# Kernel optimization log

Hardware: AMD Instinct MI355X
Metric: run time of the kernel (lower is better)

The kernel has to match this reference:

```python
import jax, jax.numpy as jnp
import numpy as np

N_NODES = 40000
N_EDGES = 640000
D_IN = 128
D_OUT = 128


def setup_inputs() -> dict:
    key = jax.random.key(0)
    k1, k2, k3 = jax.random.split(key, 3)
    x = jax.random.normal(k1, (N_NODES, D_IN), dtype=jnp.float32)
    W = jax.random.normal(k2, (D_IN, D_OUT), dtype=jnp.float32) / np.sqrt(D_IN)
    b = jnp.zeros((D_OUT,), dtype=jnp.float32)
    edge_index = jax.random.randint(k3, (2, N_EDGES), 0, N_NODES, dtype=jnp.int64)
    return {"x": x, "W": W, "b": b, "edge_index": edge_index}


def reference(x, W, b, edge_index):
    src, dst = edge_index[0], edge_index[1]
    n = x.shape[0]
    # asymmetric normalization: 1 / out-degree(src), inf -> 0
    deg = jax.ops.segment_sum(jnp.ones_like(src, dtype=x.dtype), src, num_segments=n)
    deg_inv = jnp.where(deg > 0, 1.0 / deg, 0.0)
    # GCNConv (add_self_loops=False, normalize=False): h = x @ W; msg_e = w_e * h[src_e]
    h = x @ W  # [N, D_OUT]
    msg = h[src] * deg_inv[src][:, None]  # [E, D_OUT] gather-weighted messages
    out = jax.ops.segment_sum(msg, dst, num_segments=n) + b  # scatter-add to dst
    return out
```

## Files before the change

kernel.cpp:

```cpp
#include <hip/hip_runtime.h>

#define N_NODES 40000
#define D 128
#define N_EDGES 640000
#define CAP 64
#define NSLICE 32
#define SLICE_E 20000
#define SLICE_E4 5000
#define HALF_BINS 20000
#define HALF_W 10000
#define WROW 20000
#define SRCHIST_BLKS 64
#define BIN_BLKS 625
#define GEMM_BLKS 625
#define XPAD 132

typedef __attribute__((ext_vector_type(8))) short short8_t;
typedef __attribute__((ext_vector_type(4))) float float4_t;

static __device__ __forceinline__ unsigned short f2bf(float f) {
  unsigned u = __float_as_uint(f);
  return (unsigned short)((u + 0x7fffu + ((u >> 16) & 1u)) >> 16);
}
static __device__ __forceinline__ float bf2f(unsigned short h) {
  return __uint_as_float(((unsigned)h) << 16);
}

__global__ __launch_bounds__(256) void k_prep(const float* __restrict__ W,
                                              unsigned short* __restrict__ Wb,
                                              int* __restrict__ cnt_dst) {
  const int bid = blockIdx.x;
  const int tid = threadIdx.x;
  if (bid < 64) {
    const int g = bid * 256 + tid;
    const int j = g & 7;
    const int lane = (g >> 3) & 63;
    const int q = (g >> 9) & 3;
    const int t = g >> 11;
    const int k = q * 32 + (lane >> 4) * 8 + j;
    const int d = t * 16 + (lane & 15);
    Wb[g] = f2bf(W[k * D + d]);
  } else {
    const int i = (bid - 64) * 256 + tid;
    if (i < N_NODES) cnt_dst[i] = 0;
  }
}

__global__ __launch_bounds__(256) void k_fused(
    const float* __restrict__ x, const unsigned short* __restrict__ Wb,
    const int* __restrict__ src, const int* __restrict__ dst,
    int* __restrict__ cnt_dst, unsigned* __restrict__ slabS,
    unsigned short* __restrict__ bucket, unsigned short* __restrict__ hb) {
  __shared__ unsigned smem[10240];
  const int bid = blockIdx.x;
  const int tid = threadIdx.x;

  if (bid < SRCHIST_BLKS) {
    const int b = bid >> 1;
    const int h = bid & 1;
    for (int i = tid; i < HALF_W; i += 256) smem[i] = 0;
    __syncthreads();
    const int4* p4 = (const int4*)(src + b * SLICE_E);
    const unsigned lo = (unsigned)(h * HALF_BINS);
    for (int it = tid; it < SLICE_E4; it += 256) {
      const int4 v = p4[it];
      unsigned u;
      u = (unsigned)v.x - lo; if (u < HALF_BINS) atomicAdd(&smem[u >> 1], 1u << ((u & 1) * 16));
      u = (unsigned)v.y - lo; if (u < HALF_BINS) atomicAdd(&smem[u >> 1], 1u << ((u & 1) * 16));
      u = (unsigned)v.z - lo; if (u < HALF_BINS) atomicAdd(&smem[u >> 1], 1u << ((u & 1) * 16));
      u = (unsigned)v.w - lo; if (u < HALF_BINS) atomicAdd(&smem[u >> 1], 1u << ((u & 1) * 16));
    }
    __syncthreads();
    unsigned* row = slabS + (size_t)b * WROW + h * HALF_W;
    for (int i = tid; i < HALF_W; i += 256) row[i] = smem[i];
    return;
  }

  const int t = bid - SRCHIST_BLKS;

  if (t & 1) {
    const int cid = t >> 1;
    const int e0 = (cid * 256 + tid) * 4;
    const int4 s4 = *(const int4*)(src + e0);
    const int4 d4 = *(const int4*)(dst + e0);
    int r;
    r = atomicAdd(&cnt_dst[d4.x], 1);
    if (r < CAP) bucket[(size_t)d4.x * CAP + r] = (unsigned short)s4.x;
    r = atomicAdd(&cnt_dst[d4.y], 1);
    if (r < CAP) bucket[(size_t)d4.y * CAP + r] = (unsigned short)s4.y;
    r = atomicAdd(&cnt_dst[d4.z], 1);
    if (r < CAP) bucket[(size_t)d4.z * CAP + r] = (unsigned short)s4.z;
    r = atomicAdd(&cnt_dst[d4.w], 1);
    if (r < CAP) bucket[(size_t)d4.w * CAP + r] = (unsigned short)s4.w;
    return;
  }

  const int gid = t >> 1;
  const int n0 = gid * 64;
  const int w = tid >> 6;
  const int lane = tid & 63;

  float* xl = (float*)smem;
  {
    const float4* xg = (const float4*)(x + (size_t)n0 * D);
#pragma unroll
    for (int j = 0; j < 8; ++j) {
      const int idx = tid + j * 256;
      const int row = idx >> 5;
      const int c4 = idx & 31;
      ((float4*)(xl + row * XPAD))[c4] = xg[idx];
    }
  }
  __syncthreads();

  short8_t afrag[4];
  {
    const float* ap0 = xl + (w * 16 + (lane & 15)) * XPAD + (lane >> 4) * 8;
#pragma unroll
    for (int q = 0; q < 4; ++q) {
      const float* ap = ap0 + q * 32;
      const float4 v0 = *(const float4*)ap;
      const float4 v1 = *(const float4*)(ap + 4);
      short8_t a;
      a[0] = (short)f2bf(v0.x); a[1] = (short)f2bf(v0.y);
      a[2] = (short)f2bf(v0.z); a[3] = (short)f2bf(v0.w);
      a[4] = (short)f2bf(v1.x); a[5] = (short)f2bf(v1.y);
      a[6] = (short)f2bf(v1.z); a[7] = (short)f2bf(v1.w);
      afrag[q] = a;
    }
  }

  const int orow = n0 + w * 16 + (lane >> 4) * 4;
  const int ocolbase = lane & 15;
#pragma unroll
  for (int t8 = 0; t8 < 8; ++t8) {
    float4_t acc = {0.f, 0.f, 0.f, 0.f};
#pragma unroll
    for (int q = 0; q < 4; ++q) {
      const short8_t bfrag =
          *(const short8_t*)(Wb + ((size_t)(t8 * 4 + q) * 64 + lane) * 8);
      acc = __builtin_amdgcn_mfma_f32_16x16x32_bf16(afrag[q], bfrag, acc, 0, 0, 0);
    }
    const int col = t8 * 16 + ocolbase;
#pragma unroll
    for (int r = 0; r < 4; ++r)
      hb[(size_t)(orow + r) * D + col] = f2bf(acc[r]);
  }
}

__global__ __launch_bounds__(256) void k_colsum_src(
    const unsigned* __restrict__ slabS, float* __restrict__ dinv) {
  const int w = blockIdx.x * 256 + threadIdx.x;
  if (w >= WROW) return;
  unsigned run = 0;
#pragma unroll 8
  for (int b = 0; b < NSLICE; ++b) run += slabS[(size_t)b * WROW + w];
  const unsigned lo = run & 0xFFFFu;
  const unsigned hi = run >> 16;
  dinv[2 * w] = lo ? 1.0f / (float)lo : 0.0f;
  dinv[2 * w + 1] = hi ? 1.0f / (float)hi : 0.0f;
}

__global__ __launch_bounds__(256) void k_gather(
    const int* __restrict__ cnt_dst, const float* __restrict__ dinv,
    const unsigned short* __restrict__ bucket,
    const unsigned short* __restrict__ hb,
    const float* __restrict__ b, float* __restrict__ out) {
  const int tid = threadIdx.x;
  const int node = blockIdx.x * 8 + (tid >> 5);
  const int lane = tid & 31;

  int len = cnt_dst[node];
  if (len > CAP) len = CAP;
  const unsigned short* bk = bucket + (size_t)node * CAP;

  float4 a0 = {0.f, 0.f, 0.f, 0.f};
  float4 a1 = {0.f, 0.f, 0.f, 0.f};
  float4 a2 = {0.f, 0.f, 0.f, 0.f};
  float4 a3 = {0.f, 0.f, 0.f, 0.f};

  int j = 0;
  for (; j + 3 < len; j += 4) {
    const int s0 = bk[j + 0];
    const int s1 = bk[j + 1];
    const int s2 = bk[j + 2];
    const int s3 = bk[j + 3];
    const float f0 = dinv[s0];
    const float f1 = dinv[s1];
    const float f2 = dinv[s2];
    const float f3 = dinv[s3];
    ushort4 u0 = ((const ushort4*)(hb + (size_t)s0 * D))[lane];
    ushort4 u1 = ((const ushort4*)(hb + (size_t)s1 * D))[lane];
    ushort4 u2 = ((const ushort4*)(hb + (size_t)s2 * D))[lane];
    ushort4 u3 = ((const ushort4*)(hb + (size_t)s3 * D))[lane];
    a0.x += f0 * bf2f(u0.x); a0.y += f0 * bf2f(u0.y); a0.z += f0 * bf2f(u0.z); a0.w += f0 * bf2f(u0.w);
    a1.x += f1 * bf2f(u1.x); a1.y += f1 * bf2f(u1.y); a1.z += f1 * bf2f(u1.z); a1.w += f1 * bf2f(u1.w);
    a2.x += f2 * bf2f(u2.x); a2.y += f2 * bf2f(u2.y); a2.z += f2 * bf2f(u2.z); a2.w += f2 * bf2f(u2.w);
    a3.x += f3 * bf2f(u3.x); a3.y += f3 * bf2f(u3.y); a3.z += f3 * bf2f(u3.z); a3.w += f3 * bf2f(u3.w);
  }
  for (; j < len; ++j) {
    const int s0 = bk[j];
    const float f0 = dinv[s0];
    ushort4 u0 = ((const ushort4*)(hb + (size_t)s0 * D))[lane];
    a0.x += f0 * bf2f(u0.x); a0.y += f0 * bf2f(u0.y); a0.z += f0 * bf2f(u0.z); a0.w += f0 * bf2f(u0.w);
  }

  const float4 bias = ((const float4*)b)[lane];
  float4 v;
  v.x = bias.x + (a0.x + a1.x) + (a2.x + a3.x);
  v.y = bias.y + (a0.y + a1.y) + (a2.y + a3.y);
  v.z = bias.z + (a0.z + a1.z) + (a2.z + a3.z);
  v.w = bias.w + (a0.w + a1.w) + (a2.w + a3.w);
  ((float4*)(out + (size_t)node * D))[lane] = v;
}

extern "C" void kernel_launch(void* const* d_in, const int* in_sizes, int n_in,
                              void* d_out, int out_size, void* d_ws, size_t ws_size,
                              hipStream_t stream) {
  const float* x = (const float*)d_in[0];
  const float* W = (const float*)d_in[1];
  const float* b = (const float*)d_in[2];
  const int* ei = (const int*)d_in[3];
  const int* src = ei;
  const int* dst = ei + N_EDGES;
  float* out = (float*)d_out;

  char* ws = (char*)d_ws;
  int* cnt_dst = (int*)(ws + 0);
  float* dinv = (float*)(ws + 160000);
  unsigned* slabS = (unsigned*)(ws + 320000);
  unsigned short* Wb = (unsigned short*)(ws + 2880000);
  unsigned short* bucket = (unsigned short*)(ws + 2912768);
  unsigned short* hb = (unsigned short*)(ws + 8032768);

  k_prep<<<221, 256, 0, stream>>>(W, Wb, cnt_dst);
  k_fused<<<SRCHIST_BLKS + BIN_BLKS + GEMM_BLKS, 256, 0, stream>>>(
      x, Wb, src, dst, cnt_dst, slabS, bucket, hb);
  k_colsum_src<<<79, 256, 0, stream>>>(slabS, dinv);
  k_gather<<<5000, 256, 0, stream>>>(cnt_dst, dinv, bucket, hb, b, out);
}
```

Measured before the change: 76.76 us.

## Replace global atomic dst bucketing with two-pass counting sort and LDS buckets

Replaces per-edge global atomics into a per-node bucket array with a coarse counting sort. Edges are first histogrammed per 128-node key, then prefix-scanned and scattered into a packed edge array. The gather kernel then builds each group's buckets in LDS before aggregating. This removes contended global atomics and the large bucket array, at the cost of two extra kernel launches and serialized scans. It also cuts the gather kernel's parallelism to 313 blocks that each loop over 128 nodes.

```diff
diff --git a/kernel.cpp b/kernel.cpp
--- a/kernel.cpp
+++ b/kernel.cpp
@@ -4,14 +4,17 @@
 #define D 128
 #define N_EDGES 640000
 #define CAP 64
+#define GRP 128
+#define NKEY 313
+#define P1TILE 2048
+#define P1BLKS 313
 #define NSLICE 32
 #define SLICE_E 20000
 #define SLICE_E4 5000
 #define HALF_BINS 20000
 #define HALF_W 10000
 #define WROW 20000
-#define SRCHIST_BLKS 64
-#define BIN_BLKS 625
+#define SRCH_BLKS 64
 #define GEMM_BLKS 625
 #define XPAD 132
 
@@ -26,36 +29,41 @@
   return __uint_as_float(((unsigned)h) << 16);
 }
 
+static __device__ __forceinline__ void scan512(unsigned* s, int tid) {
+  const int t2 = tid + 256;
+#pragma unroll
+  for (int off = 1; off < 512; off <<= 1) {
+    unsigned a = (tid >= off) ? s[tid - off] : 0u;
+    unsigned c = (t2 >= off) ? s[t2 - off] : 0u;
+    __syncthreads();
+    s[tid] += a;
+    s[t2] += c;
+    __syncthreads();
+  }
+}
+
 __global__ __launch_bounds__(256) void k_prep(const float* __restrict__ W,
-                                              unsigned short* __restrict__ Wb,
-                                              int* __restrict__ cnt_dst) {
-  const int bid = blockIdx.x;
-  const int tid = threadIdx.x;
-  if (bid < 64) {
-    const int g = bid * 256 + tid;
-    const int j = g & 7;
-    const int lane = (g >> 3) & 63;
-    const int q = (g >> 9) & 3;
-    const int t = g >> 11;
-    const int k = q * 32 + (lane >> 4) * 8 + j;
-    const int d = t * 16 + (lane & 15);
-    Wb[g] = f2bf(W[k * D + d]);
-  } else {
-    const int i = (bid - 64) * 256 + tid;
-    if (i < N_NODES) cnt_dst[i] = 0;
-  }
-}
-
-__global__ __launch_bounds__(256) void k_fused(
+                                              unsigned short* __restrict__ Wb) {
+  const int g = blockIdx.x * 256 + threadIdx.x;
+  const int j = g & 7;
+  const int lane = (g >> 3) & 63;
+  const int q = (g >> 9) & 3;
+  const int t = g >> 11;
+  const int k = q * 32 + (lane >> 4) * 8 + j;
+  const int d = t * 16 + (lane & 15);
+  Wb[g] = f2bf(W[k * D + d]);
+}
+
+__global__ __launch_bounds__(256) void k1(
     const float* __restrict__ x, const unsigned short* __restrict__ Wb,
     const int* __restrict__ src, const int* __restrict__ dst,
-    int* __restrict__ cnt_dst, unsigned* __restrict__ slabS,
-    unsigned short* __restrict__ bucket, unsigned short* __restrict__ hb) {
+    unsigned* __restrict__ slabS, unsigned* __restrict__ slabP,
+    unsigned short* __restrict__ hb) {
   __shared__ unsigned smem[10240];
   const int bid = blockIdx.x;
   const int tid = threadIdx.x;
 
-  if (bid < SRCHIST_BLKS) {
+  if (bid < SRCH_BLKS) {
     const int b = bid >> 1;
     const int h = bid & 1;
     for (int i = tid; i < HALF_W; i += 256) smem[i] = 0;
@@ -76,26 +84,35 @@
     return;
   }
 
-  const int t = bid - SRCHIST_BLKS;
-
-  if (t & 1) {
-    const int cid = t >> 1;
-    const int e0 = (cid * 256 + tid) * 4;
-    const int4 s4 = *(const int4*)(src + e0);
-    const int4 d4 = *(const int4*)(dst + e0);
-    int r;
-    r = atomicAdd(&cnt_dst[d4.x], 1);
-    if (r < CAP) bucket[(size_t)d4.x * CAP + r] = (unsigned short)s4.x;
-    r = atomicAdd(&cnt_dst[d4.y], 1);
-    if (r < CAP) bucket[(size_t)d4.y * CAP + r] = (unsigned short)s4.y;
-    r = atomicAdd(&cnt_dst[d4.z], 1);
-    if (r < CAP) bucket[(size_t)d4.z * CAP + r] = (unsigned short)s4.z;
-    r = atomicAdd(&cnt_dst[d4.w], 1);
-    if (r < CAP) bucket[(size_t)d4.w * CAP + r] = (unsigned short)s4.w;
+  const int t = bid - SRCH_BLKS;
+  if (t % 3 == 2) {
+    const int cid = t / 3;
+    unsigned* cnt = smem;
+    const int t2 = tid + 256;
+    if (tid < NKEY) cnt[tid] = 0;
+    if (t2 < NKEY) cnt[t2] = 0;
+    __syncthreads();
+    const int e0 = cid * P1TILE + tid * 8;
+    if (e0 < N_EDGES) {
+      const int4 da = *(const int4*)(dst + e0);
+      const int4 db = *(const int4*)(dst + e0 + 4);
+      atomicAdd(&cnt[da.x >> 7], 1u);
+      atomicAdd(&cnt[da.y >> 7], 1u);
+      atomicAdd(&cnt[da.z >> 7], 1u);
+      atomicAdd(&cnt[da.w >> 7], 1u);
+      atomicAdd(&cnt[db.x >> 7], 1u);
+      atomicAdd(&cnt[db.y >> 7], 1u);
+      atomicAdd(&cnt[db.z >> 7], 1u);
+      atomicAdd(&cnt[db.w >> 7], 1u);
+    }
+    __syncthreads();
+    if (tid < NKEY) slabP[(size_t)cid * NKEY + tid] = cnt[tid];
+    if (t2 < NKEY) slabP[(size_t)cid * NKEY + t2] = cnt[t2];
     return;
   }
 
-  const int gid = t >> 1;
+  const int gid = 2 * (t / 3) + (t % 3);
+  if (gid >= GEMM_BLKS) return;
   const int n0 = gid * 64;
   const int w = tid >> 6;
   const int lane = tid & 63;
@@ -148,9 +165,28 @@
   }
 }
 
-__global__ __launch_bounds__(256) void k_colsum_src(
-    const unsigned* __restrict__ slabS, float* __restrict__ dinv) {
-  const int w = blockIdx.x * 256 + threadIdx.x;
+__global__ __launch_bounds__(256) void k2(
+    const unsigned* __restrict__ slabP, const unsigned* __restrict__ slabS,
+    unsigned* __restrict__ rowbase, unsigned* __restrict__ keytotal,
+    float* __restrict__ dinv) {
+  const int bid = blockIdx.x;
+  const int tid = threadIdx.x;
+  if (bid < NKEY) {
+    const int k = bid;
+    __shared__ unsigned s[512];
+    const int t2 = tid + 256;
+    unsigned v0 = slabP[(size_t)tid * NKEY + k];
+    unsigned v1 = (t2 < NKEY) ? slabP[(size_t)t2 * NKEY + k] : 0u;
+    s[tid] = v0;
+    s[t2] = v1;
+    __syncthreads();
+    scan512(s, tid);
+    rowbase[(size_t)tid * NKEY + k] = s[tid] - v0;
+    if (t2 < NKEY) rowbase[(size_t)t2 * NKEY + k] = s[t2] - v1;
+    if (tid == 0) keytotal[k] = s[NKEY - 1];
+    return;
+  }
+  const int w = (bid - NKEY) * 256 + tid;
   if (w >= WROW) return;
   unsigned run = 0;
 #pragma unroll 8
@@ -161,57 +197,129 @@
   dinv[2 * w + 1] = hi ? 1.0f / (float)hi : 0.0f;
 }
 
-__global__ __launch_bounds__(256) void k_gather(
-    const int* __restrict__ cnt_dst, const float* __restrict__ dinv,
-    const unsigned short* __restrict__ bucket,
-    const unsigned short* __restrict__ hb,
-    const float* __restrict__ b, float* __restrict__ out) {
+__global__ __launch_bounds__(256) void k3(
+    const int* __restrict__ src, const int* __restrict__ dst,
+    const unsigned* __restrict__ rowbase, const unsigned* __restrict__ keytotal,
+    unsigned* __restrict__ epack) {
+  __shared__ unsigned s[512];
+  __shared__ unsigned ko[NKEY];
+  __shared__ unsigned rb[NKEY];
+  __shared__ unsigned cnt[NKEY];
+  const int b = blockIdx.x;
   const int tid = threadIdx.x;
-  const int node = blockIdx.x * 8 + (tid >> 5);
+  const int t2 = tid + 256;
+
+  unsigned kv0 = (tid < NKEY) ? keytotal[tid] : 0u;
+  unsigned kv1 = (t2 < NKEY) ? keytotal[t2] : 0u;
+  s[tid] = kv0;
+  s[t2] = kv1;
+  if (tid < NKEY) { rb[tid] = rowbase[(size_t)b * NKEY + tid]; cnt[tid] = 0; }
+  if (t2 < NKEY) { rb[t2] = rowbase[(size_t)b * NKEY + t2]; cnt[t2] = 0; }
+  __syncthreads();
+  scan512(s, tid);
+  if (tid < NKEY) ko[tid] = s[tid] - kv0;
+  if (t2 < NKEY) ko[t2] = s[t2] - kv1;
+  __syncthreads();
+
+  const int e0 = b * P1TILE + tid * 8;
+  if (e0 < N_EDGES) {
+    const int4 sa = *(const int4*)(src + e0);
+    const int4 sb = *(const int4*)(src + e0 + 4);
+    const int4 da = *(const int4*)(dst + e0);
+    const int4 db = *(const int4*)(dst + e0 + 4);
+#define PLACE(DV, SV)                                                   \
+  {                                                                     \
+    const int d_ = (DV);                                                \
+    const int k_ = d_ >> 7;                                             \
+    const unsigned lr_ = atomicAdd(&cnt[k_], 1u);                       \
+    epack[ko[k_] + rb[k_] + lr_] =                                      \
+        ((unsigned)(d_ & 127) << 16) | (unsigned)(SV);                  \
+  }
+    PLACE(da.x, sa.x) PLACE(da.y, sa.y) PLACE(da.z, sa.z) PLACE(da.w, sa.w)
+    PLACE(db.x, sb.x) PLACE(db.y, sb.y) PLACE(db.z, sb.z) PLACE(db.w, sb.w)
+#undef PLACE
+  }
+}
+
+__global__ __launch_bounds__(256) void k4(
+    const unsigned* __restrict__ keytotal, const unsigned* __restrict__ epack,
+    const float* __restrict__ dinv, const unsigned short* __restrict__ hb,
+    const float* __restrict__ bvec, float* __restrict__ out) {
+  __shared__ unsigned s[512];
+  __shared__ unsigned cnt[GRP];
+  __shared__ unsigned short bkt[GRP * CAP];
+  const int k = blockIdx.x;
+  const int tid = threadIdx.x;
+  const int t2 = tid + 256;
+
+  unsigned kv0 = (tid < NKEY) ? keytotal[tid] : 0u;
+  unsigned kv1 = (t2 < NKEY) ? keytotal[t2] : 0u;
+  s[tid] = kv0;
+  s[t2] = kv1;
+  if (tid < GRP) cnt[tid] = 0;
+  __syncthreads();
+  scan512(s, tid);
+  const unsigned start = (k > 0) ? s[k - 1] : 0u;
+  const unsigned len = s[k] - start;
+  __syncthreads();
+
+  for (unsigned i = tid; i < len; i += 256) {
+    const unsigned p = epack[start + i];
+    const unsigned dl = p >> 16;
+    const unsigned sr = p & 0xFFFFu;
+    const unsigned r = atomicAdd(&cnt[dl], 1u);
+    if (r < CAP) bkt[dl * CAP + r] = (unsigned short)sr;
+  }
+  __syncthreads();
+
   const int lane = tid & 31;
-
-  int len = cnt_dst[node];
-  if (len > CAP) len = CAP;
-  const unsigned short* bk = bucket + (size_t)node * CAP;
-
-  float4 a0 = {0.f, 0.f, 0.f, 0.f};
-  float4 a1 = {0.f, 0.f, 0.f, 0.f};
-  float4 a2 = {0.f, 0.f, 0.f, 0.f};
-  float4 a3 = {0.f, 0.f, 0.f, 0.f};
-
-  int j = 0;
-  for (; j + 3 < len; j += 4) {
-    const int s0 = bk[j + 0];
-    const int s1 = bk[j + 1];
-    const int s2 = bk[j + 2];
-    const int s3 = bk[j + 3];
-    const float f0 = dinv[s0];
-    const float f1 = dinv[s1];
-    const float f2 = dinv[s2];
-    const float f3 = dinv[s3];
-    ushort4 u0 = ((const ushort4*)(hb + (size_t)s0 * D))[lane];
-    ushort4 u1 = ((const ushort4*)(hb + (size_t)s1 * D))[lane];
-    ushort4 u2 = ((const ushort4*)(hb + (size_t)s2 * D))[lane];
-    ushort4 u3 = ((const ushort4*)(hb + (size_t)s3 * D))[lane];
-    a0.x += f0 * bf2f(u0.x); a0.y += f0 * bf2f(u0.y); a0.z += f0 * bf2f(u0.z); a0.w += f0 * bf2f(u0.w);
-    a1.x += f1 * bf2f(u1.x); a1.y += f1 * bf2f(u1.y); a1.z += f1 * bf2f(u1.z); a1.w += f1 * bf2f(u1.w);
-    a2.x += f2 * bf2f(u2.x); a2.y += f2 * bf2f(u2.y); a2.z += f2 * bf2f(u2.z); a2.w += f2 * bf2f(u2.w);
-    a3.x += f3 * bf2f(u3.x); a3.y += f3 * bf2f(u3.y); a3.z += f3 * bf2f(u3.z); a3.w += f3 * bf2f(u3.w);
-  }
-  for (; j < len; ++j) {
-    const int s0 = bk[j];
-    const float f0 = dinv[s0];
-    ushort4 u0 = ((const ushort4*)(hb + (size_t)s0 * D))[lane];
-    a0.x += f0 * bf2f(u0.x); a0.y += f0 * bf2f(u0.y); a0.z += f0 * bf2f(u0.z); a0.w += f0 * bf2f(u0.w);
-  }
-
-  const float4 bias = ((const float4*)b)[lane];
-  float4 v;
-  v.x = bias.x + (a0.x + a1.x) + (a2.x + a3.x);
-  v.y = bias.y + (a0.y + a1.y) + (a2.y + a3.y);
-  v.z = bias.z + (a0.z + a1.z) + (a2.z + a3.z);
-  v.w = bias.w + (a0.w + a1.w) + (a2.w + a3.w);
-  ((float4*)(out + (size_t)node * D))[lane] = v;
+  const int g = tid >> 5;
+  const float4 bias = ((const float4*)bvec)[lane];
+#pragma unroll 1
+  for (int c = 0; c < 16; ++c) {
+    const int nl = c * 8 + g;
+    const int n = k * GRP + nl;
+    if (n >= N_NODES) continue;
+    int ln = (int)cnt[nl];
+    if (ln > CAP) ln = CAP;
+    const unsigned short* bk = bkt + nl * CAP;
+
+    float4 a0 = {0.f, 0.f, 0.f, 0.f};
+    float4 a1 = {0.f, 0.f, 0.f, 0.f};
+    float4 a2 = {0.f, 0.f, 0.f, 0.f};
+    float4 a3 = {0.f, 0.f, 0.f, 0.f};
+    int j = 0;
+    for (; j + 3 < ln; j += 4) {
+      const int s0 = bk[j + 0];
+      const int s1 = bk[j + 1];
+      const int s2 = bk[j + 2];
+      const int s3 = bk[j + 3];
+      const float f0 = dinv[s0];
+      const float f1 = dinv[s1];
+      const float f2 = dinv[s2];
+      const float f3 = dinv[s3];
+      ushort4 u0 = ((const ushort4*)(hb + (size_t)s0 * D))[lane];
+      ushort4 u1 = ((const ushort4*)(hb + (size_t)s1 * D))[lane];
+      ushort4 u2 = ((const ushort4*)(hb + (size_t)s2 * D))[lane];
+      ushort4 u3 = ((const ushort4*)(hb + (size_t)s3 * D))[lane];
+      a0.x += f0 * bf2f(u0.x); a0.y += f0 * bf2f(u0.y); a0.z += f0 * bf2f(u0.z); a0.w += f0 * bf2f(u0.w);
+      a1.x += f1 * bf2f(u1.x); a1.y += f1 * bf2f(u1.y); a1.z += f1 * bf2f(u1.z); a1.w += f1 * bf2f(u1.w);
+      a2.x += f2 * bf2f(u2.x); a2.y += f2 * bf2f(u2.y); a2.z += f2 * bf2f(u2.z); a2.w += f2 * bf2f(u2.w);
+      a3.x += f3 * bf2f(u3.x); a3.y += f3 * bf2f(u3.y); a3.z += f3 * bf2f(u3.z); a3.w += f3 * bf2f(u3.w);
+    }
+    for (; j < ln; ++j) {
+      const int s0 = bk[j];
+      const float f0 = dinv[s0];
+      ushort4 u0 = ((const ushort4*)(hb + (size_t)s0 * D))[lane];
+      a0.x += f0 * bf2f(u0.x); a0.y += f0 * bf2f(u0.y); a0.z += f0 * bf2f(u0.z); a0.w += f0 * bf2f(u0.w);
+    }
+    float4 v;
+    v.x = bias.x + (a0.x + a1.x) + (a2.x + a3.x);
+    v.y = bias.y + (a0.y + a1.y) + (a2.y + a3.y);
+    v.z = bias.z + (a0.z + a1.z) + (a2.z + a3.z);
+    v.w = bias.w + (a0.w + a1.w) + (a2.w + a3.w);
+    ((float4*)(out + (size_t)n * D))[lane] = v;
+  }
 }
 
 extern "C" void kernel_launch(void* const* d_in, const int* in_sizes, int n_in,
@@ -226,16 +334,18 @@
   float* out = (float*)d_out;
 
   char* ws = (char*)d_ws;
-  int* cnt_dst = (int*)(ws + 0);
-  float* dinv = (float*)(ws + 160000);
-  unsigned* slabS = (unsigned*)(ws + 320000);
-  unsigned short* Wb = (unsigned short*)(ws + 2880000);
-  unsigned short* bucket = (unsigned short*)(ws + 2912768);
-  unsigned short* hb = (unsigned short*)(ws + 8032768);
-
-  k_prep<<<221, 256, 0, stream>>>(W, Wb, cnt_dst);
-  k_fused<<<SRCHIST_BLKS + BIN_BLKS + GEMM_BLKS, 256, 0, stream>>>(
-      x, Wb, src, dst, cnt_dst, slabS, bucket, hb);
-  k_colsum_src<<<79, 256, 0, stream>>>(slabS, dinv);
-  k_gather<<<5000, 256, 0, stream>>>(cnt_dst, dinv, bucket, hb, b, out);
-}
+  float* dinv = (float*)(ws + 0);
+  unsigned* slabS = (unsigned*)(ws + 160000);
+  unsigned short* Wb = (unsigned short*)(ws + 2720000);
+  unsigned* slabP = (unsigned*)(ws + 2752768);
+  unsigned* rowbase = (unsigned*)(ws + 3144704);
+  unsigned* keytotal = (unsigned*)(ws + 3536640);
+  unsigned* epack = (unsigned*)(ws + 3540992);
+  unsigned short* hb = (unsigned short*)(ws + 6100992);
+
+  k_prep<<<64, 256, 0, stream>>>(W, Wb);
+  k1<<<SRCH_BLKS + 939, 256, 0, stream>>>(x, Wb, src, dst, slabS, slabP, hb);
+  k2<<<NKEY + 79, 256, 0, stream>>>(slabP, slabS, rowbase, keytotal, dinv);
+  k3<<<P1BLKS, 256, 0, stream>>>(src, dst, rowbase, keytotal, epack);
+  k4<<<NKEY, 256, 0, stream>>>(keytotal, epack, dinv, hb, b, out);
+}
```

Result: slower. 92.84 us (+21.0%).
